# Optimization experiments

Hardware: AMD Instinct MI355X
Metric: run time of the kernel (lower is better)

Reference implementation:

```python
import jax, jax.numpy as jnp
import numpy as np

NUM_BINS = 64
BIN_WIDTH = 0.0625
X_SHAPE = (64, 4, 512, 512)  # SD-style latent batch, ~268 MB fp32


def setup_inputs() -> dict:
    key = jax.random.key(0)
    x = jax.random.normal(key, X_SHAPE, dtype=jnp.float32)
    # uniform bin centers over [-2, 2), step = BIN_WIDTH (matches init_kwargs)
    bins = (-2.0 + BIN_WIDTH * jnp.arange(NUM_BINS)).astype(jnp.float32)
    bin_width = jnp.float32(BIN_WIDTH)
    return {"x": x, "bins": bins, "bin_width": bin_width}


def reference(x, bins, bin_width):
    # out[b] = mean(0.5 - 0.5 * tanh((x - bins[b]) / bin_width * 2))
    # lax.map over the small fixed bin axis avoids materializing a
    # [num_bins, *x.shape] intermediate, matching the original's per-bin
    # streaming reduction.
    scale = 2.0 / bin_width

    def per_bin(c):
        return jnp.mean(0.5 - 0.5 * jnp.tanh((x - c) * scale))

    return jax.lax.map(per_bin, bins)  # shape [NUM_BINS]
```

## Files before the change

kernel.cpp:

```cpp
#include <hip/hip_runtime.h>
#include <hip/hip_bf16.h>


#define NCELLS (74 * 64)
#define HIST_BLOCKS 1024
#define HIST_THREADS 256

__global__ void __launch_bounds__(HIST_THREADS)
hist_kernel(const float* __restrict__ x, unsigned* __restrict__ ghist, int n)
{
    __shared__ unsigned hist[NCELLS];
    for (int i = threadIdx.x; i < NCELLS; i += HIST_THREADS) hist[i] = 0u;
    __syncthreads();

    const int n4 = n >> 2;
    const float4* __restrict__ x4 = (const float4*)x;
    const int gid    = blockIdx.x * HIST_THREADS + threadIdx.x;
    const int stride = gridDim.x * HIST_THREADS;

    for (int i = gid; i < n4; i += stride) {
        float4 v = x4[i];
        {
            int f = (int)floorf(fmaf(v.x, 1024.0f, 2368.0f));
            f = min(max(f, 0), NCELLS - 1);
            atomicAdd(&hist[f], 1u);
        }
        {
            int f = (int)floorf(fmaf(v.y, 1024.0f, 2368.0f));
            f = min(max(f, 0), NCELLS - 1);
            atomicAdd(&hist[f], 1u);
        }
        {
            int f = (int)floorf(fmaf(v.z, 1024.0f, 2368.0f));
            f = min(max(f, 0), NCELLS - 1);
            atomicAdd(&hist[f], 1u);
        }
        {
            int f = (int)floorf(fmaf(v.w, 1024.0f, 2368.0f));
            f = min(max(f, 0), NCELLS - 1);
            atomicAdd(&hist[f], 1u);
        }
    }

    if (blockIdx.x == 0) {
        int tail = n & 3;
        if (threadIdx.x < tail) {
            float v = x[n4 * 4 + threadIdx.x];
            int f = (int)floorf(fmaf(v, 1024.0f, 2368.0f));
            f = min(max(f, 0), NCELLS - 1);
            atomicAdd(&hist[f], 1u);
        }
    }

    __syncthreads();
    for (int i = threadIdx.x; i < NCELLS; i += HIST_THREADS) {
        unsigned v = hist[i];
        if (v) atomicAdd(&ghist[i], v);
    }
}

__global__ void __launch_bounds__(256)
bins_kernel(const unsigned* __restrict__ ghist, float* __restrict__ out, float invN)
{
    const int b = blockIdx.x;
    double sum = 0.0;
    for (int f = threadIdx.x; f < NCELLS; f += 256) {
        unsigned h = ghist[f];
        if (h) {
            float t = -5.0f + ((float)f + 0.5f) * (1.0f / 64.0f);
            float z = 4.0f * ((float)b - t);
            float s = 1.0f / (1.0f + __expf(-z));
            sum += (double)h * (double)s;
        }
    }
    __shared__ double sd[256];
    sd[threadIdx.x] = sum;
    __syncthreads();
    for (int ofs = 128; ofs > 0; ofs >>= 1) {
        if (threadIdx.x < ofs) sd[threadIdx.x] += sd[threadIdx.x + ofs];
        __syncthreads();
    }
    if (threadIdx.x == 0) out[b] = (float)(sd[0] * (double)invN);
}

extern "C" void kernel_launch(void* const* d_in, const int* in_sizes, int n_in,
                              void* d_out, int out_size, void* d_ws, size_t ws_size,
                              hipStream_t stream)
{
    const float* x = (const float*)d_in[0];
    const int n = in_sizes[0];
    unsigned* ghist = (unsigned*)d_ws;

    hipMemsetAsync(d_ws, 0, NCELLS * sizeof(unsigned), stream);

    hist_kernel<<<HIST_BLOCKS, HIST_THREADS, 0, stream>>>(x, ghist, n);
    bins_kernel<<<64, 256, 0, stream>>>(ghist, (float*)d_out, 1.0f / (float)n);
}
```

Before: 368.1 us.

## Fold per-block histogram into bin sums with fixed-point atomics

Each block now turns its shared histogram straight into per-bin partial sums. It uses a precomputed sigmoid window in LDS plus prefix group counts, and adds the results into 64 fixed-point 64-bit global accumulators. This removes the per-cell global atomics and the separate 64-block bins reduction. The change also moves to 512-thread blocks, unrolls the main loop by 4 with nontemporal loads, and drops floorf, which differs from floor only for negative indices that are clamped anyway. In exchange it adds per-block fold work and relies on the sigmoid window being exact for the cells beyond the window (saturated to 0 or 1).

After: 495.0 us. +34.5%, slower.

```diff
diff --git a/kernel.cpp b/kernel.cpp
--- a/kernel.cpp
+++ b/kernel.cpp
@@ -1,86 +1,108 @@
 #include <hip/hip_runtime.h>
-#include <hip/hip_bf16.h>
 
 
-#define NCELLS (74 * 64)
-#define HIST_BLOCKS 1024
-#define HIST_THREADS 256
+#define NCELLS   (74 * 64)
+#define NBINS    64
+#define NGROUPS  74
+#define WIN      640
+#define HIST_BLOCKS  1024
+#define HIST_THREADS 512
+#define FIX_SCALE 1048576.0
+
+typedef float floatv4 __attribute__((ext_vector_type(4)));
 
 __global__ void __launch_bounds__(HIST_THREADS)
-hist_kernel(const float* __restrict__ x, unsigned* __restrict__ ghist, int n)
+hist_fold_kernel(const float* __restrict__ x,
+                 unsigned long long* __restrict__ gacc, int n)
 {
     __shared__ unsigned hist[NCELLS];
-    for (int i = threadIdx.x; i < NCELLS; i += HIST_THREADS) hist[i] = 0u;
+    __shared__ float    sig[WIN];
+    __shared__ unsigned G[NGROUPS];
+    __shared__ unsigned P[NBINS];
+
+    const int tid = threadIdx.x;
+
+    for (int i = tid; i < NCELLS; i += HIST_THREADS) hist[i] = 0u;
+    for (int j = tid; j < WIN; j += HIST_THREADS) {
+        float z = (319.5f - (float)j) * 0.0625f;
+        sig[j] = 1.0f / (1.0f + __expf(-z));
+    }
     __syncthreads();
 
     const int n4 = n >> 2;
-    const float4* __restrict__ x4 = (const float4*)x;
-    const int gid    = blockIdx.x * HIST_THREADS + threadIdx.x;
+    const floatv4* __restrict__ x4 = (const floatv4*)x;
+    const int gid    = blockIdx.x * HIST_THREADS + tid;
     const int stride = gridDim.x * HIST_THREADS;
 
-    for (int i = gid; i < n4; i += stride) {
-        float4 v = x4[i];
-        {
-            int f = (int)floorf(fmaf(v.x, 1024.0f, 2368.0f));
-            f = min(max(f, 0), NCELLS - 1);
-            atomicAdd(&hist[f], 1u);
-        }
-        {
-            int f = (int)floorf(fmaf(v.y, 1024.0f, 2368.0f));
-            f = min(max(f, 0), NCELLS - 1);
-            atomicAdd(&hist[f], 1u);
-        }
-        {
-            int f = (int)floorf(fmaf(v.z, 1024.0f, 2368.0f));
-            f = min(max(f, 0), NCELLS - 1);
-            atomicAdd(&hist[f], 1u);
-        }
-        {
-            int f = (int)floorf(fmaf(v.w, 1024.0f, 2368.0f));
-            f = min(max(f, 0), NCELLS - 1);
-            atomicAdd(&hist[f], 1u);
+#define BUMP1(val) do {                                   \
+        int f = (int)fmaf((val), 1024.0f, 2368.0f);       \
+        f = min(max(f, 0), NCELLS - 1);                   \
+        atomicAdd(&hist[f], 1u);                          \
+    } while (0)
+#define BUMP4(v) do { BUMP1((v).x); BUMP1((v).y); BUMP1((v).z); BUMP1((v).w); } while (0)
+
+    int i = gid;
+    for (; i + 3 * stride < n4; i += 4 * stride) {
+        floatv4 a = __builtin_nontemporal_load(&x4[i]);
+        floatv4 b = __builtin_nontemporal_load(&x4[i + stride]);
+        floatv4 c = __builtin_nontemporal_load(&x4[i + 2 * stride]);
+        floatv4 d = __builtin_nontemporal_load(&x4[i + 3 * stride]);
+        BUMP4(a); BUMP4(b); BUMP4(c); BUMP4(d);
+    }
+    for (; i < n4; i += stride) {
+        floatv4 a = __builtin_nontemporal_load(&x4[i]);
+        BUMP4(a);
+    }
+    if (blockIdx.x == 0) {
+        int tail = n & 3;
+        if (tid < tail) { float v = x[(n4 << 2) + tid]; BUMP1(v); }
+    }
+    __syncthreads();
+
+    const int wave = tid >> 6;
+    const int lane = tid & 63;
+
+    for (int g = wave; g < NGROUPS; g += HIST_THREADS / 64) {
+        unsigned v = hist[(g << 6) + lane];
+        #pragma unroll
+        for (int o = 32; o; o >>= 1) v += __shfl_xor(v, o);
+        if (lane == 0) G[g] = v;
+    }
+    __syncthreads();
+
+    if (tid < NBINS) {
+        unsigned p = 0;
+        for (int g = 0; g < tid; ++g) p += G[g];
+        P[tid] = p;
+    }
+    __syncthreads();
+
+    #pragma unroll
+    for (int bi = 0; bi < 8; ++bi) {
+        const int b = (wave << 3) + bi;
+        float ws = 0.0f;
+        const int base = (b << 6) + lane;
+        #pragma unroll
+        for (int p = 0; p < 10; ++p)
+            ws += (float)hist[base + (p << 6)] * sig[(p << 6) + lane];
+        #pragma unroll
+        for (int o = 32; o; o >>= 1) ws += __shfl_xor(ws, o);
+        if (lane == 0) {
+            unsigned long long s = ((unsigned long long)P[b] << 20)
+                                 + (unsigned long long)((double)ws * FIX_SCALE + 0.5);
+            atomicAdd(&gacc[b], s);
         }
     }
-
-    if (blockIdx.x == 0) {
-        int tail = n & 3;
-        if (threadIdx.x < tail) {
-            float v = x[n4 * 4 + threadIdx.x];
-            int f = (int)floorf(fmaf(v, 1024.0f, 2368.0f));
-            f = min(max(f, 0), NCELLS - 1);
-            atomicAdd(&hist[f], 1u);
-        }
-    }
-
-    __syncthreads();
-    for (int i = threadIdx.x; i < NCELLS; i += HIST_THREADS) {
-        unsigned v = hist[i];
-        if (v) atomicAdd(&ghist[i], v);
-    }
+#undef BUMP1
+#undef BUMP4
 }
 
-__global__ void __launch_bounds__(256)
-bins_kernel(const unsigned* __restrict__ ghist, float* __restrict__ out, float invN)
+__global__ void __launch_bounds__(64)
+finalize_kernel(const unsigned long long* __restrict__ gacc,
+                float* __restrict__ out, double inv)
 {
-    const int b = blockIdx.x;
-    double sum = 0.0;
-    for (int f = threadIdx.x; f < NCELLS; f += 256) {
-        unsigned h = ghist[f];
-        if (h) {
-            float t = -5.0f + ((float)f + 0.5f) * (1.0f / 64.0f);
-            float z = 4.0f * ((float)b - t);
-            float s = 1.0f / (1.0f + __expf(-z));
-            sum += (double)h * (double)s;
-        }
-    }
-    __shared__ double sd[256];
-    sd[threadIdx.x] = sum;
-    __syncthreads();
-    for (int ofs = 128; ofs > 0; ofs >>= 1) {
-        if (threadIdx.x < ofs) sd[threadIdx.x] += sd[threadIdx.x + ofs];
-        __syncthreads();
-    }
-    if (threadIdx.x == 0) out[b] = (float)(sd[0] * (double)invN);
+    const int b = threadIdx.x;
+    out[b] = (float)((double)gacc[b] * inv);
 }
 
 extern "C" void kernel_launch(void* const* d_in, const int* in_sizes, int n_in,
@@ -89,10 +111,11 @@
 {
     const float* x = (const float*)d_in[0];
     const int n = in_sizes[0];
-    unsigned* ghist = (unsigned*)d_ws;
+    unsigned long long* gacc = (unsigned long long*)d_ws;
 
-    hipMemsetAsync(d_ws, 0, NCELLS * sizeof(unsigned), stream);
+    (void)hipMemsetAsync(d_ws, 0, NBINS * sizeof(unsigned long long), stream);
 
-    hist_kernel<<<HIST_BLOCKS, HIST_THREADS, 0, stream>>>(x, ghist, n);
-    bins_kernel<<<64, 256, 0, stream>>>(ghist, (float*)d_out, 1.0f / (float)n);
+    hist_fold_kernel<<<HIST_BLOCKS, HIST_THREADS, 0, stream>>>(x, gacc, n);
+    finalize_kernel<<<1, 64, 0, stream>>>(gacc, (float*)d_out,
+                                          1.0 / ((double)n * FIX_SCALE));
 }
```
